# Kernel tuning notes

Hardware: AMD Instinct MI355X
Metric: run time of the kernel (lower is better)

Reference implementation:

```python
import jax, jax.numpy as jnp
import numpy as np

B, S, D = 4, 2048, 1024  # batch, seq_len, input_dim == output_dim (dk)


def setup_inputs() -> dict:
    key = jax.random.key(0)
    kx, kq, kk, kv = jax.random.split(key, 4)
    # xavier_uniform bound for square [D, D] matrices
    bound = float(np.sqrt(6.0 / (D + D)))
    return {
        "x": jax.random.normal(kx, (B, S, D), dtype=jnp.float32),
        "WQ": jax.random.uniform(kq, (D, D), jnp.float32, -bound, bound),
        "WK": jax.random.uniform(kk, (D, D), jnp.float32, -bound, bound),
        "WV": jax.random.uniform(kv, (D, D), jnp.float32, -bound, bound),
    }


def reference(x, WQ, WK, WV):
    dk = WQ.shape[1]
    q = x @ WQ  # [B, S, dk]
    k = x @ WK
    v = x @ WV
    scores = jnp.einsum("bsd,btd->bst", q, k) / jnp.sqrt(jnp.asarray(dk, x.dtype))
    # causal mask: tril ones -> positions where mask==0 set to -inf
    s = x.shape[1]
    causal = jnp.tril(jnp.ones((s, s), dtype=bool))
    scores = jnp.where(causal[None, :, :], scores, jnp.asarray(-jnp.inf, x.dtype))
    attention = jax.nn.softmax(scores, axis=-1)
    # NOTE: original applies attention_dropout to `scores` post-softmax and
    # discards the result -> dead op; eval-mode output is attention @ v.
    return jnp.einsum("bst,btd->bsd", attention, v)
```

## Files before the change

kernel.cpp:

```cpp
#include <hip/hip_runtime.h>
#include <stdint.h>


typedef unsigned short u16;
typedef __attribute__((ext_vector_type(8))) short shortx8;
typedef __attribute__((ext_vector_type(4))) float floatx4;

static constexpr int BB = 4;
static constexpr int SS = 2048;
static constexpr int DD = 1024;

__device__ __forceinline__ u16 f2bf(float f) {
  union { float f; uint32_t u; } c; c.f = f;
  uint32_t u = c.u;
  return (u16)((u + 0x7fffu + ((u >> 16) & 1u)) >> 16);
}

#define GLOAD_LDS16(g, l)                                                              \
  __builtin_amdgcn_global_load_lds((const __attribute__((address_space(1))) void*)(g), \
                                   (__attribute__((address_space(3))) void*)(l), 16, 0, 0)

__device__ __forceinline__ void gemm_core_128(
    const u16* __restrict__ A, const u16* __restrict__ Bt,
    int lda, int ldb, int m0, int n0, int kend, floatx4 acc[4][4])
{
  __shared__ u16 lA[128 * 64];
  __shared__ u16 lB[128 * 64];
  const int t = threadIdx.x;
  const int w = t >> 6, l = t & 63;
  const int wm = w >> 1, wn = w & 1;
  const int sr = l >> 3;
  const int sc = (l & 7) * 8;

#pragma unroll
  for (int i = 0; i < 4; ++i)
#pragma unroll
    for (int j = 0; j < 4; ++j)
      acc[i][j] = (floatx4){0.f, 0.f, 0.f, 0.f};

  const u16* Ab = A + (size_t)m0 * lda;
  const u16* Bb = Bt + (size_t)n0 * ldb;

  for (int k0 = 0; k0 < kend; k0 += 64) {
#pragma unroll
    for (int i = 0; i < 4; ++i) {
      const int row = w * 32 + i * 8;
      GLOAD_LDS16(Ab + (size_t)(row + sr) * lda + k0 + sc, &lA[row * 64]);
      GLOAD_LDS16(Bb + (size_t)(row + sr) * ldb + k0 + sc, &lB[row * 64]);
    }
    __syncthreads();

#pragma unroll
    for (int ks = 0; ks < 2; ++ks) {
      shortx8 af[4], bf[4];
#pragma unroll
      for (int i = 0; i < 4; ++i)
        af[i] = *(const shortx8*)&lA[(wm * 64 + i * 16 + (l & 15)) * 64 + ks * 32 + (l >> 4) * 8];
#pragma unroll
      for (int i = 0; i < 4; ++i)
        bf[i] = *(const shortx8*)&lB[(wn * 64 + i * 16 + (l & 15)) * 64 + ks * 32 + (l >> 4) * 8];
#pragma unroll
      for (int i = 0; i < 4; ++i)
#pragma unroll
        for (int j = 0; j < 4; ++j)
          acc[i][j] = __builtin_amdgcn_mfma_f32_16x16x32_bf16(af[i], bf[j], acc[i][j], 0, 0, 0);
    }
    __syncthreads();
  }
}

__global__ __launch_bounds__(256) void prep(const float* __restrict__ x,
                                            const float* __restrict__ WQ,
                                            const float* __restrict__ WK,
                                            const float* __restrict__ WV,
                                            u16* __restrict__ xb,
                                            u16* __restrict__ Wt) {
  __shared__ float tile[64][65];
  const int bid = blockIdx.x;
  const int t = threadIdx.x;
  if (bid < 8192) {
    const size_t i = (size_t)bid * 256 + t;
    float4 v = ((const float4*)x)[i];
    ushort4 o;
    o.x = f2bf(v.x); o.y = f2bf(v.y); o.z = f2bf(v.z); o.w = f2bf(v.w);
    ((ushort4*)xb)[i] = o;
    return;
  }
  const int r = bid - 8192;
  const int wsel = r >> 8;
  const int rr = r & 255;
  const int k0 = (rr >> 4) * 64, n0 = (rr & 15) * 64;
  const float* W = wsel == 0 ? WQ : (wsel == 1 ? WK : WV);
  const int tx = t & 63, ty = t >> 6;
#pragma unroll
  for (int i = 0; i < 16; ++i)
    tile[ty + i * 4][tx] = W[(size_t)(k0 + ty + i * 4) * DD + n0 + tx];
  __syncthreads();
  u16* dst = Wt + (size_t)wsel * DD * DD;
#pragma unroll
  for (int i = 0; i < 16; ++i)
    dst[(size_t)(n0 + ty + i * 4) * DD + k0 + tx] = f2bf(tile[tx][ty + i * 4]);
}

__global__ __launch_bounds__(256, 2) void qkv_gemm(const u16* __restrict__ x,
                                                   const u16* __restrict__ Wt,
                                                   u16* __restrict__ Q,
                                                   u16* __restrict__ K,
                                                   u16* __restrict__ Vt) {
  const int m0 = blockIdx.x * 128;
  const int n0t = blockIdx.y * 128;
  floatx4 acc[4][4];
  gemm_core_128(x, Wt, DD, DD, m0, n0t, DD, acc);

  const int t = threadIdx.x, w = t >> 6, l = t & 63;
  const int wm = w >> 1, wn = w & 1;

  if (n0t >= 2048) {
    const int bb = m0 >> 11;
    const int s0 = (m0 & 2047) + wm * 64 + (l >> 4) * 4;
    u16* vt = Vt + (size_t)bb * DD * SS;
#pragma unroll
    for (int i = 0; i < 4; ++i)
#pragma unroll
      for (int j = 0; j < 4; ++j) {
        const int n = (n0t - 2048) + wn * 64 + j * 16 + (l & 15);
        const int s = s0 + i * 16;
        ushort4 o4;
        o4.x = f2bf(acc[i][j][0]);
        o4.y = f2bf(acc[i][j][1]);
        o4.z = f2bf(acc[i][j][2]);
        o4.w = f2bf(acc[i][j][3]);
        *(ushort4*)(vt + (size_t)n * SS + s) = o4;
      }
    return;
  }

  u16* out = (n0t < 1024) ? Q : K;
  const int n0 = n0t & 1023;
#pragma unroll
  for (int i = 0; i < 4; ++i)
#pragma unroll
    for (int j = 0; j < 4; ++j)
#pragma unroll
      for (int r = 0; r < 4; ++r) {
        const int m = m0 + wm * 64 + i * 16 + (l >> 4) * 4 + r;
        const int n = n0 + wn * 64 + j * 16 + (l & 15);
        out[(size_t)m * DD + n] = f2bf(acc[i][j][r]);
      }
}

__global__ __launch_bounds__(256, 2) void scores_gemm(const u16* __restrict__ Q,
                                                      const u16* __restrict__ Kt,
                                                      float* __restrict__ Sc) {
  const int b = blockIdx.z;
  const int tcode = blockIdx.x;
  int mb = (int)((sqrtf(8.0f * (float)tcode + 1.0f) - 1.0f) * 0.5f);
  while ((mb + 1) * (mb + 2) / 2 <= tcode) ++mb;
  while (mb * (mb + 1) / 2 > tcode) --mb;
  const int nb = tcode - mb * (mb + 1) / 2;
  const int m0 = mb * 128, n0 = nb * 128;

  floatx4 acc[4][4];
  gemm_core_128(Q + (size_t)b * SS * DD, Kt + (size_t)b * SS * DD, DD, DD, m0, n0, DD, acc);

  float* out = Sc + (size_t)b * SS * SS;
  const int t = threadIdx.x, w = t >> 6, l = t & 63;
  const int wm = w >> 1, wn = w & 1;
#pragma unroll
  for (int i = 0; i < 4; ++i)
#pragma unroll
    for (int j = 0; j < 4; ++j)
#pragma unroll
      for (int r = 0; r < 4; ++r) {
        const int m = m0 + wm * 64 + i * 16 + (l >> 4) * 4 + r;
        const int n = n0 + wn * 64 + j * 16 + (l & 15);
        out[(size_t)m * SS + n] = acc[i][j][r] * 0.03125f;
      }
}

__global__ __launch_bounds__(256) void softmax_causal(const float* __restrict__ Sc,
                                                      u16* __restrict__ P) {
  const int row = blockIdx.x * 4 + (threadIdx.x >> 6);
  const int l = threadIdx.x & 63;
  const int b = row >> 11, i = row & 2047;
  const float* s = Sc + (size_t)b * SS * SS + (size_t)i * SS;
  u16* p = P + (size_t)b * SS * SS + (size_t)i * SS;
  const int n = i + 1;
  const int jend = (i + 128) & ~127;
  const int nc = (jend + 255) >> 8;

  float4 v[8];
  float mx = -INFINITY;
#pragma unroll
  for (int c = 0; c < 8; ++c) {
    if (c < nc) {
      const int col = (c * 64 + l) * 4;
      float4 a = *(const float4*)(s + col);
      a.x = (col + 0 < n) ? a.x : -INFINITY;
      a.y = (col + 1 < n) ? a.y : -INFINITY;
      a.z = (col + 2 < n) ? a.z : -INFINITY;
      a.w = (col + 3 < n) ? a.w : -INFINITY;
      v[c] = a;
      mx = fmaxf(mx, fmaxf(fmaxf(a.x, a.y), fmaxf(a.z, a.w)));
    }
  }
#pragma unroll
  for (int o = 32; o > 0; o >>= 1) mx = fmaxf(mx, __shfl_xor(mx, o, 64));

  float sum = 0.f;
#pragma unroll
  for (int c = 0; c < 8; ++c) {
    if (c < nc) {
      float4 a = v[c];
      a.x = __expf(a.x - mx);
      a.y = __expf(a.y - mx);
      a.z = __expf(a.z - mx);
      a.w = __expf(a.w - mx);
      v[c] = a;
      sum += (a.x + a.y) + (a.z + a.w);
    }
  }
#pragma unroll
  for (int o = 32; o > 0; o >>= 1) sum += __shfl_xor(sum, o, 64);
  const float inv = 1.0f / sum;

#pragma unroll
  for (int c = 0; c < 8; ++c) {
    if (c < nc) {
      const int col = (c * 64 + l) * 4;
      ushort4 o4;
      o4.x = f2bf(v[c].x * inv);
      o4.y = f2bf(v[c].y * inv);
      o4.z = f2bf(v[c].z * inv);
      o4.w = f2bf(v[c].w * inv);
      *(ushort4*)(p + col) = o4;
    }
  }
}

__global__ __launch_bounds__(256, 2) void pv_gemm(const u16* __restrict__ P,
                                                  const u16* __restrict__ Vt,
                                                  float* __restrict__ out) {
  const int b = blockIdx.z;
  const int mb = 15 - blockIdx.y;
  const int m0 = mb * 128, n0 = blockIdx.x * 128;
  floatx4 acc[4][4];
  gemm_core_128(P + (size_t)b * SS * SS, Vt + (size_t)b * DD * SS, SS, SS, m0, n0, m0 + 128, acc);

  float* o = out + (size_t)b * SS * DD;
  const int t = threadIdx.x, w = t >> 6, l = t & 63;
  const int wm = w >> 1, wn = w & 1;
#pragma unroll
  for (int i = 0; i < 4; ++i)
#pragma unroll
    for (int j = 0; j < 4; ++j)
#pragma unroll
      for (int r = 0; r < 4; ++r) {
        const int m = m0 + wm * 64 + i * 16 + (l >> 4) * 4 + r;
        const int n = n0 + wn * 64 + j * 16 + (l & 15);
        o[(size_t)m * DD + n] = acc[i][j][r];
      }
}

extern "C" void kernel_launch(void* const* d_in, const int* in_sizes, int n_in,
                              void* d_out, int out_size, void* d_ws, size_t ws_size,
                              hipStream_t stream) {
  const float* x  = (const float*)d_in[0];
  const float* WQ = (const float*)d_in[1];
  const float* WK = (const float*)d_in[2];
  const float* WV = (const float*)d_in[3];
  float* out = (float*)d_out;

  char* ws = (char*)d_ws;
  const size_t WT_OFF = 0;
  const size_t XB_OFF = WT_OFF + (size_t)3072 * 1024 * 2;
  const size_t Q_OFF  = XB_OFF + (size_t)BB * SS * DD * 2;
  const size_t K_OFF  = Q_OFF + (size_t)BB * SS * DD * 2;
  const size_t VT_OFF = K_OFF + (size_t)BB * SS * DD * 2;
  const size_t P_OFF  = VT_OFF + (size_t)BB * SS * DD * 2;
  const size_t SC_OFF = P_OFF + (size_t)BB * SS * SS * 2;
  u16*   Wt = (u16*)(ws + WT_OFF);
  u16*   xb = (u16*)(ws + XB_OFF);
  u16*   Q  = (u16*)(ws + Q_OFF);
  u16*   Kb = (u16*)(ws + K_OFF);
  u16*   Vt = (u16*)(ws + VT_OFF);
  u16*   P  = (u16*)(ws + P_OFF);
  float* Sc = (float*)(ws + SC_OFF);

  hipLaunchKernelGGL(prep, dim3(8960), dim3(256), 0, stream, x, WQ, WK, WV, xb, Wt);
  hipLaunchKernelGGL(qkv_gemm, dim3(64, 24), dim3(256), 0, stream, xb, Wt, Q, Kb, Vt);
  hipLaunchKernelGGL(scores_gemm, dim3(136, 1, 4), dim3(256), 0, stream, Q, Kb, Sc);
  hipLaunchKernelGGL(softmax_causal, dim3(2048), dim3(256), 0, stream, Sc, P);
  hipLaunchKernelGGL(pv_gemm, dim3(8, 16, 4), dim3(256), 0, stream, P, Vt, out);
}
```

Before: 262.8 us.

## Store scores as bf16 and XOR-swizzle LDS tiles in shared GEMM core

The scores GEMM now writes bf16 instead of fp32, and softmax reads 8 bf16 values per lane, halving scores traffic on both the write and read side. The shared GEMM core XOR-swizzles the 16-byte column chunks when loading into LDS and when reading fragments, to avoid LDS bank conflicts. Softmax also skips stores past the causal block boundary. Rounding scores to bf16 before softmax costs some accuracy.

```diff
diff --git a/kernel.cpp b/kernel.cpp
--- a/kernel.cpp
+++ b/kernel.cpp
@@ -14,6 +14,13 @@
   union { float f; uint32_t u; } c; c.f = f;
   uint32_t u = c.u;
   return (u16)((u + 0x7fffu + ((u >> 16) & 1u)) >> 16);
+}
+
+__device__ __forceinline__ float bfhi2f(uint32_t u) {
+  union { uint32_t u; float f; } c; c.u = u & 0xffff0000u; return c.f;
+}
+__device__ __forceinline__ float bflo2f(uint32_t u) {
+  union { uint32_t u; float f; } c; c.u = u << 16; return c.f;
 }
 
 #define GLOAD_LDS16(g, l)                                                              \
@@ -30,7 +37,7 @@
   const int w = t >> 6, l = t & 63;
   const int wm = w >> 1, wn = w & 1;
   const int sr = l >> 3;
-  const int sc = (l & 7) * 8;
+  const int scq = ((l & 7) ^ (l >> 3)) * 8;
 
 #pragma unroll
   for (int i = 0; i < 4; ++i)
@@ -45,20 +52,21 @@
 #pragma unroll
     for (int i = 0; i < 4; ++i) {
       const int row = w * 32 + i * 8;
-      GLOAD_LDS16(Ab + (size_t)(row + sr) * lda + k0 + sc, &lA[row * 64]);
-      GLOAD_LDS16(Bb + (size_t)(row + sr) * ldb + k0 + sc, &lB[row * 64]);
+      GLOAD_LDS16(Ab + (size_t)(row + sr) * lda + k0 + scq, &lA[row * 64]);
+      GLOAD_LDS16(Bb + (size_t)(row + sr) * ldb + k0 + scq, &lB[row * 64]);
     }
     __syncthreads();
 
 #pragma unroll
     for (int ks = 0; ks < 2; ++ks) {
+      const int ca = ((ks * 4 + (l >> 4)) ^ (l & 7)) * 8;
       shortx8 af[4], bf[4];
 #pragma unroll
       for (int i = 0; i < 4; ++i)
-        af[i] = *(const shortx8*)&lA[(wm * 64 + i * 16 + (l & 15)) * 64 + ks * 32 + (l >> 4) * 8];
+        af[i] = *(const shortx8*)&lA[(wm * 64 + i * 16 + (l & 15)) * 64 + ca];
 #pragma unroll
       for (int i = 0; i < 4; ++i)
-        bf[i] = *(const shortx8*)&lB[(wn * 64 + i * 16 + (l & 15)) * 64 + ks * 32 + (l >> 4) * 8];
+        bf[i] = *(const shortx8*)&lB[(wn * 64 + i * 16 + (l & 15)) * 64 + ca];
 #pragma unroll
       for (int i = 0; i < 4; ++i)
 #pragma unroll
@@ -151,7 +159,7 @@
 
 __global__ __launch_bounds__(256, 2) void scores_gemm(const u16* __restrict__ Q,
                                                       const u16* __restrict__ Kt,
-                                                      float* __restrict__ Sc) {
+                                                      u16* __restrict__ Scb) {
   const int b = blockIdx.z;
   const int tcode = blockIdx.x;
   int mb = (int)((sqrtf(8.0f * (float)tcode + 1.0f) - 1.0f) * 0.5f);
@@ -163,7 +171,7 @@
   floatx4 acc[4][4];
   gemm_core_128(Q + (size_t)b * SS * DD, Kt + (size_t)b * SS * DD, DD, DD, m0, n0, DD, acc);
 
-  float* out = Sc + (size_t)b * SS * SS;
+  u16* out = Scb + (size_t)b * SS * SS;
   const int t = threadIdx.x, w = t >> 6, l = t & 63;
   const int wm = w >> 1, wn = w & 1;
 #pragma unroll
@@ -174,34 +182,37 @@
       for (int r = 0; r < 4; ++r) {
         const int m = m0 + wm * 64 + i * 16 + (l >> 4) * 4 + r;
         const int n = n0 + wn * 64 + j * 16 + (l & 15);
-        out[(size_t)m * SS + n] = acc[i][j][r] * 0.03125f;
-      }
-}
-
-__global__ __launch_bounds__(256) void softmax_causal(const float* __restrict__ Sc,
+        out[(size_t)m * SS + n] = f2bf(acc[i][j][r] * 0.03125f);
+      }
+}
+
+__global__ __launch_bounds__(256) void softmax_causal(const u16* __restrict__ Scb,
                                                       u16* __restrict__ P) {
   const int row = blockIdx.x * 4 + (threadIdx.x >> 6);
   const int l = threadIdx.x & 63;
   const int b = row >> 11, i = row & 2047;
-  const float* s = Sc + (size_t)b * SS * SS + (size_t)i * SS;
+  const u16* s = Scb + (size_t)b * SS * SS + (size_t)i * SS;
   u16* p = P + (size_t)b * SS * SS + (size_t)i * SS;
   const int n = i + 1;
   const int jend = (i + 128) & ~127;
-  const int nc = (jend + 255) >> 8;
-
-  float4 v[8];
+  const int nc = (jend + 511) >> 9;
+
+  float v[4][8];
   float mx = -INFINITY;
 #pragma unroll
-  for (int c = 0; c < 8; ++c) {
+  for (int c = 0; c < 4; ++c) {
     if (c < nc) {
-      const int col = (c * 64 + l) * 4;
-      float4 a = *(const float4*)(s + col);
-      a.x = (col + 0 < n) ? a.x : -INFINITY;
-      a.y = (col + 1 < n) ? a.y : -INFINITY;
-      a.z = (col + 2 < n) ? a.z : -INFINITY;
-      a.w = (col + 3 < n) ? a.w : -INFINITY;
-      v[c] = a;
-      mx = fmaxf(mx, fmaxf(fmaxf(a.x, a.y), fmaxf(a.z, a.w)));
+      const int col = c * 512 + l * 8;
+      uint4 raw = *(const uint4*)(s + col);
+      v[c][0] = bflo2f(raw.x); v[c][1] = bfhi2f(raw.x);
+      v[c][2] = bflo2f(raw.y); v[c][3] = bfhi2f(raw.y);
+      v[c][4] = bflo2f(raw.z); v[c][5] = bfhi2f(raw.z);
+      v[c][6] = bflo2f(raw.w); v[c][7] = bfhi2f(raw.w);
+#pragma unroll
+      for (int e = 0; e < 8; ++e) {
+        v[c][e] = (col + e < n) ? v[c][e] : -INFINITY;
+        mx = fmaxf(mx, v[c][e]);
+      }
     }
   }
 #pragma unroll
@@ -209,15 +220,13 @@
 
   float sum = 0.f;
 #pragma unroll
-  for (int c = 0; c < 8; ++c) {
+  for (int c = 0; c < 4; ++c) {
     if (c < nc) {
-      float4 a = v[c];
-      a.x = __expf(a.x - mx);
-      a.y = __expf(a.y - mx);
-      a.z = __expf(a.z - mx);
-      a.w = __expf(a.w - mx);
-      v[c] = a;
-      sum += (a.x + a.y) + (a.z + a.w);
+#pragma unroll
+      for (int e = 0; e < 8; ++e) {
+        v[c][e] = __expf(v[c][e] - mx);
+        sum += v[c][e];
+      }
     }
   }
 #pragma unroll
@@ -225,15 +234,17 @@
   const float inv = 1.0f / sum;
 
 #pragma unroll
-  for (int c = 0; c < 8; ++c) {
+  for (int c = 0; c < 4; ++c) {
     if (c < nc) {
-      const int col = (c * 64 + l) * 4;
-      ushort4 o4;
-      o4.x = f2bf(v[c].x * inv);
-      o4.y = f2bf(v[c].y * inv);
-      o4.z = f2bf(v[c].z * inv);
-      o4.w = f2bf(v[c].w * inv);
-      *(ushort4*)(p + col) = o4;
+      const int col = c * 512 + l * 8;
+      if (col < jend) {
+        uint4 o4;
+        o4.x = (uint32_t)f2bf(v[c][0] * inv) | ((uint32_t)f2bf(v[c][1] * inv) << 16);
+        o4.y = (uint32_t)f2bf(v[c][2] * inv) | ((uint32_t)f2bf(v[c][3] * inv) << 16);
+        o4.z = (uint32_t)f2bf(v[c][4] * inv) | ((uint32_t)f2bf(v[c][5] * inv) << 16);
+        o4.w = (uint32_t)f2bf(v[c][6] * inv) | ((uint32_t)f2bf(v[c][7] * inv) << 16);
+        *(uint4*)(p + col) = o4;
+      }
     }
   }
 }
@@ -279,17 +290,17 @@
   const size_t VT_OFF = K_OFF + (size_t)BB * SS * DD * 2;
   const size_t P_OFF  = VT_OFF + (size_t)BB * SS * DD * 2;
   const size_t SC_OFF = P_OFF + (size_t)BB * SS * SS * 2;
-  u16*   Wt = (u16*)(ws + WT_OFF);
-  u16*   xb = (u16*)(ws + XB_OFF);
-  u16*   Q  = (u16*)(ws + Q_OFF);
-  u16*   Kb = (u16*)(ws + K_OFF);
-  u16*   Vt = (u16*)(ws + VT_OFF);
-  u16*   P  = (u16*)(ws + P_OFF);
-  float* Sc = (float*)(ws + SC_OFF);
+  u16* Wt  = (u16*)(ws + WT_OFF);
+  u16* xb  = (u16*)(ws + XB_OFF);
+  u16* Q   = (u16*)(ws + Q_OFF);
+  u16* Kb  = (u16*)(ws + K_OFF);
+  u16* Vt  = (u16*)(ws + VT_OFF);
+  u16* P   = (u16*)(ws + P_OFF);
+  u16* Scb = (u16*)(ws + SC_OFF);
 
   hipLaunchKernelGGL(prep, dim3(8960), dim3(256), 0, stream, x, WQ, WK, WV, xb, Wt);
   hipLaunchKernelGGL(qkv_gemm, dim3(64, 24), dim3(256), 0, stream, xb, Wt, Q, Kb, Vt);
-  hipLaunchKernelGGL(scores_gemm, dim3(136, 1, 4), dim3(256), 0, stream, Q, Kb, Sc);
-  hipLaunchKernelGGL(softmax_causal, dim3(2048), dim3(256), 0, stream, Sc, P);
+  hipLaunchKernelGGL(scores_gemm, dim3(136, 1, 4), dim3(256), 0, stream, Q, Kb, Scb);
+  hipLaunchKernelGGL(softmax_causal, dim3(2048), dim3(256), 0, stream, Scb, P);
   hipLaunchKernelGGL(pv_gemm, dim3(8, 16, 4), dim3(256), 0, stream, P, Vt, out);
 }
```

Result: faster. 236.6 us (-10.0%).
